# Kernel tuning notes

Hardware: AMD Instinct MI355X
Metric: run time of the kernel (lower is better)

The kernel has to match this reference:

```python
import jax, jax.numpy as jnp
import numpy as np

N, E, F, DH, R = 50000, 800000, 128, 128, 6  # nodes, edges, in-feat, hidden, relations (heads=1)
EPS = 1e-5
NEG_SLOPE = 0.01


def setup_inputs() -> dict:
    key = jax.random.key(0)
    ks = jax.random.split(key, 20)
    sF = 1.0 / np.sqrt(F)
    sD = 1.0 / np.sqrt(DH)
    return {
        "x": jax.random.normal(ks[0], (N, F), dtype=jnp.float32),
        "edge_index": jax.random.randint(ks[1], (2, E), 0, N, dtype=jnp.int64),
        "edge_type": jax.random.randint(ks[2], (E,), 0, R, dtype=jnp.int64),
        # RGCNConv params
        "rgcn_w": jax.random.normal(ks[3], (R, F, DH), dtype=jnp.float32) * sF,
        "rgcn_root": jax.random.normal(ks[4], (F, DH), dtype=jnp.float32) * sF,
        "rgcn_bias": jnp.zeros((DH,), dtype=jnp.float32),
        # TransformerConv params (heads=1, concat=True)
        "wq": jax.random.normal(ks[5], (DH, DH), dtype=jnp.float32) * sD,
        "bq": jnp.zeros((DH,), dtype=jnp.float32),
        "wk": jax.random.normal(ks[6], (DH, DH), dtype=jnp.float32) * sD,
        "bk": jnp.zeros((DH,), dtype=jnp.float32),
        "wv": jax.random.normal(ks[7], (DH, DH), dtype=jnp.float32) * sD,
        "bv": jnp.zeros((DH,), dtype=jnp.float32),
        "wskip": jax.random.normal(ks[8], (DH, DH), dtype=jnp.float32) * sD,
        "bskip": jnp.zeros((DH,), dtype=jnp.float32),
        # BatchNorm1d params (training-mode batch stats)
        "bn_gamma": jnp.ones((DH,), dtype=jnp.float32),
        "bn_beta": jnp.zeros((DH,), dtype=jnp.float32),
    }


def _rgcn(x, src, dst, edge_type, w, root, bias):
    # PyG RGCNConv: per-relation mean aggregation of x_j @ W_r over incoming edges, + root + bias
    out = x @ root + bias  # [N, DH]
    for r in range(R):
        m = (edge_type == r)
        xw = x @ w[r]  # [N, DH]
        msg = jnp.where(m[:, None], xw[src], 0.0)  # [E, DH]
        s = jax.ops.segment_sum(msg, dst, num_segments=N)
        cnt = jax.ops.segment_sum(m.astype(x.dtype), dst, num_segments=N)
        out = out + s / jnp.maximum(cnt, 1.0)[:, None]
    return out


def _transformer_conv(x, src, dst, wq, bq, wk, bk, wv, bv, wskip, bskip):
    # PyG TransformerConv, heads=1: edge-softmax attention over incoming edges + skip projection
    q = x @ wq + bq  # [N, DH]
    k = x @ wk + bk
    v = x @ wv + bv
    score = jnp.sum(q[dst] * k[src], axis=-1) / jnp.sqrt(jnp.asarray(DH, x.dtype))  # [E]
    smax = jax.ops.segment_max(score, dst, num_segments=N)  # -inf for empty segments (unused)
    a = jnp.exp(score - smax[dst])
    denom = jax.ops.segment_sum(a, dst, num_segments=N)
    alpha = a / denom[dst]  # every edge's dst has >=1 edge, denom > 0
    agg = jax.ops.segment_sum(alpha[:, None] * v[src], dst, num_segments=N)  # [N, DH]
    return agg + (x @ wskip + bskip)


def reference(x, edge_index, edge_type, rgcn_w, rgcn_root, rgcn_bias,
              wq, bq, wk, bk, wv, bv, wskip, bskip, bn_gamma, bn_beta):
    src, dst = edge_index[0], edge_index[1]
    h = _rgcn(x, src, dst, edge_type, rgcn_w, rgcn_root, rgcn_bias)
    h = _transformer_conv(h, src, dst, wq, bq, wk, bk, wv, bv, wskip, bskip)
    # BatchNorm1d (training: batch statistics, biased variance)
    mu = jnp.mean(h, axis=0)
    var = jnp.mean(jnp.square(h - mu), axis=0)
    h = bn_gamma * (h - mu) * jax.lax.rsqrt(var + EPS) + bn_beta
    return jnp.where(h > 0, h, NEG_SLOPE * h)
```

## Files before the change

kernel.cpp:

```cpp
#include <hip/hip_runtime.h>
#include <hip/hip_bf16.h>
#include <math.h>

#define FDIM 128
#define NREL 6

typedef _Float16 half8 __attribute__((ext_vector_type(8)));
typedef _Float16 h16x2 __attribute__((ext_vector_type(2)));
typedef float f32x4 __attribute__((ext_vector_type(4)));

#if __has_builtin(__builtin_amdgcn_fdot2)
#define FDOT2(A, B, C) __builtin_amdgcn_fdot2((A), (B), (C), false)
#else
#define FDOT2(A, B, C) ((float)(A)[0] * (float)(B)[0] + ((float)(A)[1] * (float)(B)[1] + (C)))
#endif

static __device__ __forceinline__ unsigned short f2h(float f) {
  union { _Float16 h; unsigned short u; } p; p.h = (_Float16)f; return p.u;
}

__global__ void cvt_x_kernel(const float* __restrict__ x, unsigned short* __restrict__ xh,
                             int n4) {
  int i = blockIdx.x * 256 + threadIdx.x;
  if (i < n4) {
    float4 v = ((const float4*)x)[i];
    union { _Float16 h[4]; uint2 u; } p;
    p.h[0] = (_Float16)v.x; p.h[1] = (_Float16)v.y;
    p.h[2] = (_Float16)v.z; p.h[3] = (_Float16)v.w;
    ((uint2*)xh)[i] = p.u;
  }
}

__global__ void cvt_wr_kernel(const float* __restrict__ root, const float* __restrict__ w,
                              unsigned short* __restrict__ bt) {
  int i = blockIdx.x * 256 + threadIdx.x;
  if (i < 896 * 128) {
    int n = i / 896, kk = i - n * 896;
    float v = (kk < 128) ? root[kk * 128 + n] : w[(long long)(kk - 128) * 128 + n];
    bt[i] = f2h(v);
  }
}

struct WPtrs { const float* W[4]; };
__global__ void cvt_wq_kernel(WPtrs wp, unsigned short* __restrict__ bt) {
  int i = blockIdx.x * 256 + threadIdx.x;
  if (i < 4 * 128 * 128) {
    int z = i >> 14;
    int r = i & 16383;
    int n = r >> 7, kk = r & 127;
    bt[i] = f2h(wp.W[z][kk * 128 + n]);
  }
}

struct GArgs {
  const unsigned short* Ax;
  const unsigned short* Aagg;
  const unsigned short* Bt;
  const float* bias[4];
  unsigned short* qh; unsigned short* kh; unsigned short* vh; float* sk;
  unsigned short* h;
  int M, K;
};

template <int MODE>
__launch_bounds__(256)
__global__ void gemm_mfma(GArgs g) {
  __shared__ unsigned short Ah[64 * 64];
  __shared__ unsigned short Bh[128 * 64];
  const int tid = threadIdx.x;
  const int lane = tid & 63;
  const int wid = tid >> 6;
  const int wm = wid >> 1, wn = wid & 1;
  const int lr = lane & 15, lk = lane >> 4;
  const int m0 = blockIdx.x * 64;
  const int z = (MODE == 1) ? blockIdx.z : 0;
  const unsigned short* Bt = g.Bt + (long long)z * 128 * g.K;
  const int K = g.K;
  const int M = g.M;

  f32x4 acc[2][4];
#pragma unroll
  for (int a = 0; a < 2; ++a)
#pragma unroll
    for (int b = 0; b < 4; ++b) { acc[a][b][0] = 0.f; acc[a][b][1] = 0.f; acc[a][b][2] = 0.f; acc[a][b][3] = 0.f; }

  for (int k0 = 0; k0 < K; k0 += 64) {
    __syncthreads();
#pragma unroll
    for (int p = 0; p < 2; ++p) {
      int idx = tid + 256 * p;
      int r = idx >> 3, c = idx & 7;
      int row = m0 + r; if (row > M - 1) row = M - 1;
      const unsigned short* srcp;
      if (MODE == 0)
        srcp = (k0 < 128) ? (g.Ax + (long long)row * 128 + k0 + c * 8)
                          : (g.Aagg + (long long)row * 768 + (k0 - 128) + c * 8);
      else
        srcp = g.Ax + (long long)row * 128 + k0 + c * 8;
      uint4 u = *(const uint4*)srcp;
      ((uint4*)Ah)[r * 8 + (c ^ (r & 7))] = u;
    }
#pragma unroll
    for (int p = 0; p < 4; ++p) {
      int idx = tid + 256 * p;
      int rn = idx >> 3, c = idx & 7;
      uint4 u = *(const uint4*)(Bt + (long long)rn * K + k0 + c * 8);
      ((uint4*)Bh)[rn * 8 + (c ^ (rn & 7))] = u;
    }
    __syncthreads();
#pragma unroll
    for (int ks = 0; ks < 2; ++ks) {
      half8 a[2], b[4];
#pragma unroll
      for (int fm = 0; fm < 2; ++fm) {
        int row = wm * 32 + fm * 16 + lr;
        a[fm] = *(const half8*)&((uint4*)Ah)[row * 8 + ((ks * 4 + lk) ^ (row & 7))];
      }
#pragma unroll
      for (int fn = 0; fn < 4; ++fn) {
        int col = wn * 64 + fn * 16 + lr;
        b[fn] = *(const half8*)&((uint4*)Bh)[col * 8 + ((ks * 4 + lk) ^ (col & 7))];
      }
#pragma unroll
      for (int fm = 0; fm < 2; ++fm)
#pragma unroll
        for (int fn = 0; fn < 4; ++fn)
          acc[fm][fn] = __builtin_amdgcn_mfma_f32_16x16x32_f16(a[fm], b[fn], acc[fm][fn], 0, 0, 0);
    }
  }

  const float CF = 0.08838834764831845f * 1.4426950408889634f;
  const float* bias = (MODE == 0) ? g.bias[0] : g.bias[z];
#pragma unroll
  for (int fm = 0; fm < 2; ++fm) {
#pragma unroll
    for (int fn = 0; fn < 4; ++fn) {
      int col = wn * 64 + fn * 16 + lr;
      float bv = bias[col];
#pragma unroll
      for (int j = 0; j < 4; ++j) {
        int row = m0 + wm * 32 + fm * 16 + lk * 4 + j;
        if (row < M) {
          float vv = acc[fm][fn][j] + bv;
          long long off = (long long)row * 128 + col;
          if (MODE == 0) {
            g.h[off] = f2h(vv);
          } else {
            if (z == 0) g.qh[off] = f2h(vv * CF);
            else if (z == 1) g.kh[off] = f2h(vv);
            else if (z == 2) g.vh[off] = f2h(vv);
            else g.sk[off] = vv;
          }
        }
      }
    }
  }
}

__global__ void hist_kernel(const int* __restrict__ dst, const int* __restrict__ etype,
                            int* __restrict__ cnt, int E) {
  int e = blockIdx.x * blockDim.x + threadIdx.x;
  if (e < E) atomicAdd(&cnt[dst[e] * NREL + etype[e]], 1);
}

__launch_bounds__(1024)
__global__ void scan1(const int* __restrict__ deg, int* __restrict__ incl,
                      int* __restrict__ part, int n) {
  __shared__ int sh[1024];
  int tid = threadIdx.x;
  int i = blockIdx.x * 1024 + tid;
  sh[tid] = (i < n) ? deg[i] : 0;
  __syncthreads();
  for (int o = 1; o < 1024; o <<= 1) {
    int t = (tid >= o) ? sh[tid - o] : 0;
    __syncthreads();
    sh[tid] += t;
    __syncthreads();
  }
  if (i < n) incl[i] = sh[tid];
  if (tid == 1023) part[blockIdx.x] = sh[1023];
}

__global__ void scan2(int* part, int nb) {
  int lane = threadIdx.x;
  int run = 0;
  for (int b0 = 0; b0 < nb; b0 += 64) {
    int i = b0 + lane;
    int orig = (i < nb) ? part[i] : 0;
    int v = orig;
#pragma unroll
    for (int o = 1; o < 64; o <<= 1) {
      int t = __shfl_up(v, o);
      if (lane >= o) v += t;
    }
    if (i < nb) part[i] = run + v - orig;
    run += __shfl(v, 63);
  }
}

__global__ void scan3(const int* __restrict__ incl, const int* __restrict__ part,
                      int* __restrict__ offs, int n) {
  int i = blockIdx.x * blockDim.x + threadIdx.x;
  if (i < n) {
    offs[i + 1] = incl[i] + part[i >> 10];
    if (i == 0) offs[0] = 0;
  }
}

__global__ void scatter_kernel(const int* __restrict__ src, const int* __restrict__ dst,
                               const int* __restrict__ etype, const int* __restrict__ offs6,
                               int* __restrict__ cur, int* __restrict__ csrc, int E) {
  int e = blockIdx.x * blockDim.x + threadIdx.x;
  if (e < E) {
    int key = dst[e] * NREL + etype[e];
    int p = offs6[key] + atomicAdd(&cur[key], 1);
    csrc[p] = src[e] << 8;
  }
}

__launch_bounds__(256)
__global__ void rgcn_agg(const unsigned short* __restrict__ xh, const int* __restrict__ offs6,
                         const int* __restrict__ csrc,
                         unsigned short* __restrict__ aggh, int N) {
  int node = blockIdx.x * 4 + (threadIdx.x >> 6);
  if (node >= N) return;
  int lane = threadIdx.x & 63;
  const char* xc = (const char*)xh;
  const int* bp = offs6 + node * NREL;
  const int b0 = bp[0];
  int bn0 = bp[1], bn1 = bp[2], bn2 = bp[3], bn3 = bp[4], bn4 = bp[5], bn5 = bp[6];
  const int b6 = bn5;
  unsigned* ap = (unsigned*)(aggh + (long long)node * (NREL * FDIM)) + lane;

  float tx = 0.f, ty = 0.f;
  float px = 0.f, py = 0.f;
  int bprev = b0, snaps = 0;

#define FLUSH(EPOS)                                                          \
  while (snaps < NREL && bn0 == (EPOS)) {                                    \
    int cnt_ = (EPOS) - bprev;                                               \
    float inv_ = cnt_ ? 1.f / (float)cnt_ : 0.f;                             \
    union { _Float16 h[2]; unsigned u; } pk_;                                \
    pk_.h[0] = (_Float16)((tx - px) * inv_);                                 \
    pk_.h[1] = (_Float16)((ty - py) * inv_);                                 \
    *ap = pk_.u; ap += 64;                                                   \
    px = tx; py = ty; bprev = (EPOS); ++snaps;                               \
    bn0 = bn1; bn1 = bn2; bn2 = bn3; bn3 = bn4; bn4 = bn5;                   \
  }

#define EAT(XU)                                                              \
  {                                                                          \
    union { unsigned u; _Float16 h[2]; } c_; c_.u = (XU);                    \
    tx += (float)c_.h[0]; ty += (float)c_.h[1];                              \
  }

  FLUSH(b0)
  int e = b0;
  for (; e + 16 <= b6; e += 16) {
    unsigned xv[16];
#pragma unroll
    for (int t = 0; t < 16; ++t)
      xv[t] = ((const unsigned*)(xc + csrc[e + t]))[lane];
    EAT(xv[0])  FLUSH(e + 1)   EAT(xv[1])  FLUSH(e + 2)
    EAT(xv[2])  FLUSH(e + 3)   EAT(xv[3])  FLUSH(e + 4)
    EAT(xv[4])  FLUSH(e + 5)   EAT(xv[5])  FLUSH(e + 6)
    EAT(xv[6])  FLUSH(e + 7)   EAT(xv[7])  FLUSH(e + 8)
    EAT(xv[8])  FLUSH(e + 9)   EAT(xv[9])  FLUSH(e + 10)
    EAT(xv[10]) FLUSH(e + 11)  EAT(xv[11]) FLUSH(e + 12)
    EAT(xv[12]) FLUSH(e + 13)  EAT(xv[13]) FLUSH(e + 14)
    EAT(xv[14]) FLUSH(e + 15)  EAT(xv[15]) FLUSH(e + 16)
  }
  for (; e + 4 <= b6; e += 4) {
    unsigned y0 = ((const unsigned*)(xc + csrc[e + 0]))[lane];
    unsigned y1 = ((const unsigned*)(xc + csrc[e + 1]))[lane];
    unsigned y2 = ((const unsigned*)(xc + csrc[e + 2]))[lane];
    unsigned y3 = ((const unsigned*)(xc + csrc[e + 3]))[lane];
    EAT(y0) FLUSH(e + 1) EAT(y1) FLUSH(e + 2)
    EAT(y2) FLUSH(e + 3) EAT(y3) FLUSH(e + 4)
  }
  for (; e < b6; ++e) {
    unsigned xv = ((const unsigned*)(xc + csrc[e]))[lane];
    EAT(xv) FLUSH(e + 1)
  }
#undef EAT
#undef FLUSH
}

__launch_bounds__(256)
__global__ void attn_kernel(const unsigned short* __restrict__ qh,
                            const unsigned short* __restrict__ kh,
                            const unsigned short* __restrict__ vh,
                            const int* __restrict__ offs6, const int* __restrict__ csrc,
                            float* __restrict__ out,
                            float* __restrict__ gsumB, float* __restrict__ gsqB, int N) {
  __shared__ float bsum[4][FDIM];
  __shared__ float bsq[4][FDIM];
  int wv = threadIdx.x >> 6;
  int node = blockIdx.x * 4 + wv;
  int lane = threadIdx.x & 63;
  bool active = (node < N);
  int start = 0, end = 0;
  if (active) { start = offs6[node * NREL]; end = offs6[node * NREL + NREL]; }
  int deg = end - start;

  const int g16 = lane >> 4;
  const int f = lane & 15;
  const char* kc = (const char*)kh;
  const char* vc = (const char*)vh;

  union U4 { uint4 u; h16x2 h[4]; };
  U4 qf;
  if (active) qf.u = *(const uint4*)(qh + (long long)node * FDIM + f * 8);

  float m = -INFINITY, den = 0.f, acc0 = 0.f, acc1 = 0.f;

#define LOADQ(E0, S0, S1, S2, S3, KU, V0, V1, V2, V3)                        \
  {                                                                          \
    S0 = csrc[(E0) + (g16 ^ 0)];                                             \
    S1 = csrc[(E0) + (g16 ^ 1)];                                             \
    S2 = csrc[(E0) + (g16 ^ 2)];                                             \
    S3 = csrc[(E0) + (g16 ^ 3)];                                             \
    KU = *(const uint4*)(kc + S0 + f * 16);                                  \
    V0 = ((const unsigned*)(vc + S0))[lane];                                 \
    V1 = ((const unsigned*)(vc + S1))[lane];                                 \
    V2 = ((const unsigned*)(vc + S2))[lane];                                 \
    V3 = ((const unsigned*)(vc + S3))[lane];                                 \
  }

#define PROCESS(KU, V0, V1, V2, V3, MASKED, M0, M1, M2, M3)                  \
  {                                                                          \
    U4 kf; kf.u = KU;                                                        \
    float pd = FDOT2(qf.h[0], kf.h[0], 0.f);                                 \
    pd = FDOT2(qf.h[1], kf.h[1], pd);                                        \
    pd = FDOT2(qf.h[2], kf.h[2], pd);                                        \
    pd = FDOT2(qf.h[3], kf.h[3], pd);                                        \
    pd += __shfl_xor(pd, 1);  pd += __shfl_xor(pd, 2);                       \
    pd += __shfl_xor(pd, 4);  pd += __shfl_xor(pd, 8);                       \
    float sc0 = pd;                                                          \
    float sc1 = __shfl_xor(pd, 16);                                          \
    float sc2 = __shfl_xor(pd, 32);                                          \
    float sc3 = __shfl_xor(pd, 48);                                          \
    if (MASKED) {                                                            \
      if (!(M0)) sc0 = -INFINITY;                                            \
      if (!(M1)) sc1 = -INFINITY;                                            \
      if (!(M2)) sc2 = -INFINITY;                                            \
      if (!(M3)) sc3 = -INFINITY;                                            \
    }                                                                        \
    float mx = fmaxf(fmaxf(sc0, sc1), fmaxf(sc2, sc3));                      \
    float mn = fmaxf(m, mx);                                                 \
    float scl = exp2f(m - mn);                                               \
    float a0 = exp2f(sc0 - mn), a1 = exp2f(sc1 - mn);                        \
    float a2 = exp2f(sc2 - mn), a3 = exp2f(sc3 - mn);                        \
    den = den * scl + ((a0 + a1) + (a2 + a3));                               \
    union { unsigned u; _Float16 h[2]; } w0, w1, w2, w3;                     \
    w0.u = V0; w1.u = V1; w2.u = V2; w3.u = V3;                              \
    acc0 = acc0 * scl + a0 * (float)w0.h[0] + a1 * (float)w1.h[0]            \
                      + a2 * (float)w2.h[0] + a3 * (float)w3.h[0];           \
    acc1 = acc1 * scl + a0 * (float)w0.h[1] + a1 * (float)w1.h[1]            \
                      + a2 * (float)w2.h[1] + a3 * (float)w3.h[1];           \
    m = mn;                                                                  \
  }

  if (deg > 0) {
    int nfull4 = deg & ~3;
    int e = start;
    if (nfull4 > 0) {
      int sA0, sA1, sA2, sA3; uint4 kA; unsigned vA0, vA1, vA2, vA3;
      LOADQ(e, sA0, sA1, sA2, sA3, kA, vA0, vA1, vA2, vA3)
      for (; e < start + nfull4; e += 4) {
        int sB0, sB1, sB2, sB3; uint4 kB; unsigned vB0, vB1, vB2, vB3;
        bool more = (e + 4 < start + nfull4);
        if (more) LOADQ(e + 4, sB0, sB1, sB2, sB3, kB, vB0, vB1, vB2, vB3)
        PROCESS(kA, vA0, vA1, vA2, vA3, false, 1, 1, 1, 1)
        if (more) { kA = kB; vA0 = vB0; vA1 = vB1; vA2 = vB2; vA3 = vB3; }
      }
    }
    int rem = deg & 3;
    if (rem) {
      int e0 = start + nfull4;
      int j0 = g16 ^ 0, j1 = g16 ^ 1, j2 = g16 ^ 2, j3 = g16 ^ 3;
      int sT0 = csrc[e0 + (j0 < rem ? j0 : 0)];
      int sT1 = csrc[e0 + (j1 < rem ? j1 : 0)];
      int sT2 = csrc[e0 + (j2 < rem ? j2 : 0)];
      int sT3 = csrc[e0 + (j3 < rem ? j3 : 0)];
      uint4 kT = *(const uint4*)(kc + sT0 + f * 16);
      unsigned vT0 = ((const unsigned*)(vc + sT0))[lane];
      unsigned vT1 = ((const unsigned*)(vc + sT1))[lane];
      unsigned vT2 = ((const unsigned*)(vc + sT2))[lane];
      unsigned vT3 = ((const unsigned*)(vc + sT3))[lane];
      PROCESS(kT, vT0, vT1, vT2, vT3, true, j0 < rem, j1 < rem, j2 < rem, j3 < rem)
    }
  }
#undef LOADQ
#undef PROCESS

  float2 o = make_float2(0.f, 0.f);
  if (active) {
    float2* op = (float2*)(out + (long long)node * FDIM);
    o = op[lane];
    if (deg > 0) {
      float inv = 1.f / den;
      o.x += acc0 * inv;
      o.y += acc1 * inv;
      op[lane] = o;
    }
  }

  ((float2*)bsum[wv])[lane] = make_float2(o.x, o.y);
  ((float2*)bsq[wv])[lane]  = make_float2(o.x * o.x, o.y * o.y);
  __syncthreads();
  if (threadIdx.x < FDIM) {
    int d = threadIdx.x;
    float s  = bsum[0][d] + bsum[1][d] + bsum[2][d] + bsum[3][d];
    float q2 = bsq[0][d]  + bsq[1][d]  + bsq[2][d]  + bsq[3][d];
    int bucket = blockIdx.x & 31;
    atomicAdd(&gsumB[bucket * FDIM + d], s);
    atomicAdd(&gsqB[bucket * FDIM + d], q2);
  }
}

__global__ void bn_final(const float* __restrict__ gsumB, const float* __restrict__ gsqB,
                         const float* __restrict__ gamma, const float* __restrict__ beta,
                         float* __restrict__ ss, int N) {
  int d = threadIdx.x;
  if (d < FDIM) {
    float s = 0.f, q = 0.f;
    for (int b = 0; b < 32; ++b) { s += gsumB[b * FDIM + d]; q += gsqB[b * FDIM + d]; }
    float mean = s / (float)N;
    float var = q / (float)N - mean * mean;
    var = fmaxf(var, 0.f);
    float sc = gamma[d] * rsqrtf(var + 1e-5f);
    ss[d] = sc;
    ss[FDIM + d] = beta[d] - mean * sc;
  }
}

__global__ void bn_apply(float* __restrict__ x, const float* __restrict__ ss, long long total4) {
  long long i = (long long)blockIdx.x * blockDim.x + threadIdx.x;
  if (i < total4) {
    int d0 = (int)((i * 4) & (FDIM - 1));
    float4 vv = ((const float4*)x)[i];
    float y0 = ss[d0 + 0] * vv.x + ss[FDIM + d0 + 0];
    float y1 = ss[d0 + 1] * vv.y + ss[FDIM + d0 + 1];
    float y2 = ss[d0 + 2] * vv.z + ss[FDIM + d0 + 2];
    float y3 = ss[d0 + 3] * vv.w + ss[FDIM + d0 + 3];
    vv.x = (y0 > 0.f) ? y0 : 0.01f * y0;
    vv.y = (y1 > 0.f) ? y1 : 0.01f * y1;
    vv.z = (y2 > 0.f) ? y2 : 0.01f * y2;
    vv.w = (y3 > 0.f) ? y3 : 0.01f * y3;
    ((float4*)x)[i] = vv;
  }
}

extern "C" void kernel_launch(void* const* d_in, const int* in_sizes, int n_in,
                              void* d_out, int out_size, void* d_ws, size_t ws_size,
                              hipStream_t stream) {
  const float* x         = (const float*)d_in[0];
  const int*   ei        = (const int*)d_in[1];
  const int*   etype     = (const int*)d_in[2];
  const float* rgcn_w    = (const float*)d_in[3];
  const float* rgcn_root = (const float*)d_in[4];
  const float* rgcn_bias = (const float*)d_in[5];
  const float* wq = (const float*)d_in[6];  const float* bq = (const float*)d_in[7];
  const float* wk = (const float*)d_in[8];  const float* bk = (const float*)d_in[9];
  const float* wv = (const float*)d_in[10]; const float* bv = (const float*)d_in[11];
  const float* wsk = (const float*)d_in[12]; const float* bsk = (const float*)d_in[13];
  const float* gamma = (const float*)d_in[14]; const float* beta = (const float*)d_in[15];

  const int N = in_sizes[0] / FDIM;
  const int E = in_sizes[1] / 2;
  const int* src = ei;
  const int* dst = ei + E;
  const int NK = N * NREL;

  char* base = (char*)d_ws;
  size_t off = 0;
  auto alloc = [&](size_t bytes) -> char* {
    char* p = base + off;
    off += (bytes + 255) & ~(size_t)255;
    return p;
  };
  unsigned short* aggh = (unsigned short*)alloc((size_t)N * (NREL * FDIM) * 2);
  unsigned short* qbuf = aggh;
  unsigned short* kbuf = aggh + (size_t)N * FDIM;
  unsigned short* vbuf = aggh + 2 * (size_t)N * FDIM;
  unsigned short* xh   = (unsigned short*)alloc((size_t)N * FDIM * 2);
  unsigned short* hh   = (unsigned short*)alloc((size_t)N * FDIM * 2);
  unsigned short* btR  = (unsigned short*)alloc((size_t)896 * 128 * 2);
  unsigned short* btQ  = (unsigned short*)alloc((size_t)4 * 128 * 128 * 2);
  int* cnt6 = (int*)alloc((size_t)2 * NK * 4);
  int* cur  = cnt6 + NK;
  int* offs6 = (int*)alloc((size_t)(NK + 1) * 4);
  int* incl = (int*)alloc((size_t)NK * 4);
  int* part = (int*)alloc((size_t)512 * 4);
  int* csrc = (int*)alloc((size_t)E * 4);
  float* gsumB = (float*)alloc((size_t)32 * FDIM * 4);
  float* gsqB  = (float*)alloc((size_t)32 * FDIM * 4);
  float* ss    = (float*)alloc((size_t)2 * FDIM * 4);

  float* out = (float*)d_out;

  hipMemsetAsync(cnt6, 0, (size_t)2 * NK * sizeof(int), stream);
  hipMemsetAsync(gsumB, 0, (size_t)64 * FDIM * sizeof(float), stream);

  int n4 = N * FDIM / 4;
  cvt_x_kernel<<<(n4 + 255) / 256, 256, 0, stream>>>(x, xh, n4);
  cvt_wr_kernel<<<(896 * 128 + 255) / 256, 256, 0, stream>>>(rgcn_root, rgcn_w, btR);
  WPtrs wp; wp.W[0] = wq; wp.W[1] = wk; wp.W[2] = wv; wp.W[3] = wsk;
  cvt_wq_kernel<<<(4 * 128 * 128 + 255) / 256, 256, 0, stream>>>(wp, btQ);

  hist_kernel<<<(E + 255) / 256, 256, 0, stream>>>(dst, etype, cnt6, E);
  int nb = (NK + 1023) / 1024;
  scan1<<<nb, 1024, 0, stream>>>(cnt6, incl, part, NK);
  scan2<<<1, 64, 0, stream>>>(part, nb);
  scan3<<<(NK + 255) / 256, 256, 0, stream>>>(incl, part, offs6, NK);
  scatter_kernel<<<(E + 255) / 256, 256, 0, stream>>>(src, dst, etype, offs6, cur, csrc, E);

  const int nodeBlocks = (N + 3) / 4;
  const int gemmBlocks = (N + 63) / 64;

  rgcn_agg<<<nodeBlocks, 256, 0, stream>>>(xh, offs6, csrc, aggh, N);

  GArgs g0 = {};
  g0.Ax = xh; g0.Aagg = aggh; g0.Bt = btR;
  g0.bias[0] = rgcn_bias;
  g0.h = hh; g0.M = N; g0.K = 896;
  gemm_mfma<0><<<dim3(gemmBlocks, 1, 1), 256, 0, stream>>>(g0);

  GArgs g1 = {};
  g1.Ax = hh; g1.Bt = btQ;
  g1.bias[0] = bq; g1.bias[1] = bk; g1.bias[2] = bv; g1.bias[3] = bsk;
  g1.qh = qbuf; g1.kh = kbuf; g1.vh = vbuf; g1.sk = out;
  g1.M = N; g1.K = 128;
  gemm_mfma<1><<<dim3(gemmBlocks, 1, 4), 256, 0, stream>>>(g1);

  attn_kernel<<<nodeBlocks, 256, 0, stream>>>(qbuf, kbuf, vbuf, offs6, csrc, out,
                                              gsumB, gsqB, N);

  bn_final<<<1, 128, 0, stream>>>(gsumB, gsqB, gamma, beta, ss, N);
  long long total4 = (long long)N * FDIM / 4;
  bn_apply<<<(int)((total4 + 255) / 256), 256, 0, stream>>>(out, ss, total4);
}
```

Baseline: 305.2 us.

## Interleave K and V rows, merge weight conversions, use fp16 attention accumulation

K and V projections are written into one interleaved buffer with 512-byte rows, so each gathered source node's key and value sit in the same memory region. The three conversion kernels are merged into one launch. The CSR source list now stores raw indices, and each consumer shifts them to its own row stride. The attention value accumulator switches from two fp32 scalars to a packed fp16 pair, which cuts ALU work at the cost of accuracy and a possible overflow risk in the running sum.

```diff
diff --git a/kernel.cpp b/kernel.cpp
--- a/kernel.cpp
+++ b/kernel.cpp
@@ -19,36 +19,34 @@
   union { _Float16 h; unsigned short u; } p; p.h = (_Float16)f; return p.u;
 }
 
-__global__ void cvt_x_kernel(const float* __restrict__ x, unsigned short* __restrict__ xh,
-                             int n4) {
+struct WPtrs { const float* W[4]; };
+
+__global__ void cvt_all_kernel(const float* __restrict__ x, unsigned short* __restrict__ xh,
+                               const float* __restrict__ root, const float* __restrict__ w,
+                               unsigned short* __restrict__ btR,
+                               WPtrs wp, unsigned short* __restrict__ btQ, int n4x) {
   int i = blockIdx.x * 256 + threadIdx.x;
-  if (i < n4) {
+  if (i < n4x) {
     float4 v = ((const float4*)x)[i];
     union { _Float16 h[4]; uint2 u; } p;
     p.h[0] = (_Float16)v.x; p.h[1] = (_Float16)v.y;
     p.h[2] = (_Float16)v.z; p.h[3] = (_Float16)v.w;
     ((uint2*)xh)[i] = p.u;
-  }
-}
-
-__global__ void cvt_wr_kernel(const float* __restrict__ root, const float* __restrict__ w,
-                              unsigned short* __restrict__ bt) {
-  int i = blockIdx.x * 256 + threadIdx.x;
-  if (i < 896 * 128) {
-    int n = i / 896, kk = i - n * 896;
+    return;
+  }
+  int j = i - n4x;
+  if (j < 896 * 128) {
+    int n = j / 896, kk = j - n * 896;
     float v = (kk < 128) ? root[kk * 128 + n] : w[(long long)(kk - 128) * 128 + n];
-    bt[i] = f2h(v);
-  }
-}
-
-struct WPtrs { const float* W[4]; };
-__global__ void cvt_wq_kernel(WPtrs wp, unsigned short* __restrict__ bt) {
-  int i = blockIdx.x * 256 + threadIdx.x;
-  if (i < 4 * 128 * 128) {
-    int z = i >> 14;
-    int r = i & 16383;
+    btR[j] = f2h(v);
+    return;
+  }
+  int q = j - 896 * 128;
+  if (q < 4 * 128 * 128) {
+    int z = q >> 14;
+    int r = q & 16383;
     int n = r >> 7, kk = r & 127;
-    bt[i] = f2h(wp.W[z][kk * 128 + n]);
+    btQ[q] = f2h(wp.W[z][kk * 128 + n]);
   }
 }
 
@@ -57,7 +55,7 @@
   const unsigned short* Aagg;
   const unsigned short* Bt;
   const float* bias[4];
-  unsigned short* qh; unsigned short* kh; unsigned short* vh; float* sk;
+  unsigned short* qh; unsigned short* kv; float* sk;
   unsigned short* h;
   int M, K;
 };
@@ -142,14 +140,13 @@
         int row = m0 + wm * 32 + fm * 16 + lk * 4 + j;
         if (row < M) {
           float vv = acc[fm][fn][j] + bv;
-          long long off = (long long)row * 128 + col;
           if (MODE == 0) {
-            g.h[off] = f2h(vv);
+            g.h[(long long)row * 128 + col] = f2h(vv);
           } else {
-            if (z == 0) g.qh[off] = f2h(vv * CF);
-            else if (z == 1) g.kh[off] = f2h(vv);
-            else if (z == 2) g.vh[off] = f2h(vv);
-            else g.sk[off] = vv;
+            if (z == 0) g.qh[(long long)row * 128 + col] = f2h(vv * CF);
+            else if (z == 1) g.kv[(long long)row * 256 + col] = f2h(vv);
+            else if (z == 2) g.kv[(long long)row * 256 + 128 + col] = f2h(vv);
+            else g.sk[(long long)row * 128 + col] = vv;
           }
         }
       }
@@ -214,7 +211,7 @@
   if (e < E) {
     int key = dst[e] * NREL + etype[e];
     int p = offs6[key] + atomicAdd(&cur[key], 1);
-    csrc[p] = src[e] << 8;
+    csrc[p] = src[e];
   }
 }
 
@@ -260,7 +257,7 @@
     unsigned xv[16];
 #pragma unroll
     for (int t = 0; t < 16; ++t)
-      xv[t] = ((const unsigned*)(xc + csrc[e + t]))[lane];
+      xv[t] = ((const unsigned*)(xc + ((long long)csrc[e + t] << 8)))[lane];
     EAT(xv[0])  FLUSH(e + 1)   EAT(xv[1])  FLUSH(e + 2)
     EAT(xv[2])  FLUSH(e + 3)   EAT(xv[3])  FLUSH(e + 4)
     EAT(xv[4])  FLUSH(e + 5)   EAT(xv[5])  FLUSH(e + 6)
@@ -271,15 +268,15 @@
     EAT(xv[14]) FLUSH(e + 15)  EAT(xv[15]) FLUSH(e + 16)
   }
   for (; e + 4 <= b6; e += 4) {
-    unsigned y0 = ((const unsigned*)(xc + csrc[e + 0]))[lane];
-    unsigned y1 = ((const unsigned*)(xc + csrc[e + 1]))[lane];
-    unsigned y2 = ((const unsigned*)(xc + csrc[e + 2]))[lane];
-    unsigned y3 = ((const unsigned*)(xc + csrc[e + 3]))[lane];
+    unsigned y0 = ((const unsigned*)(xc + ((long long)csrc[e + 0] << 8)))[lane];
+    unsigned y1 = ((const unsigned*)(xc + ((long long)csrc[e + 1] << 8)))[lane];
+    unsigned y2 = ((const unsigned*)(xc + ((long long)csrc[e + 2] << 8)))[lane];
+    unsigned y3 = ((const unsigned*)(xc + ((long long)csrc[e + 3] << 8)))[lane];
     EAT(y0) FLUSH(e + 1) EAT(y1) FLUSH(e + 2)
     EAT(y2) FLUSH(e + 3) EAT(y3) FLUSH(e + 4)
   }
   for (; e < b6; ++e) {
-    unsigned xv = ((const unsigned*)(xc + csrc[e]))[lane];
+    unsigned xv = ((const unsigned*)(xc + ((long long)csrc[e] << 8)))[lane];
     EAT(xv) FLUSH(e + 1)
   }
 #undef EAT
@@ -288,8 +285,7 @@
 
 __launch_bounds__(256)
 __global__ void attn_kernel(const unsigned short* __restrict__ qh,
-                            const unsigned short* __restrict__ kh,
-                            const unsigned short* __restrict__ vh,
+                            const unsigned short* __restrict__ kv,
                             const int* __restrict__ offs6, const int* __restrict__ csrc,
                             float* __restrict__ out,
                             float* __restrict__ gsumB, float* __restrict__ gsqB, int N) {
@@ -305,26 +301,26 @@
 
   const int g16 = lane >> 4;
   const int f = lane & 15;
-  const char* kc = (const char*)kh;
-  const char* vc = (const char*)vh;
+  const char* kvc = (const char*)kv;
 
   union U4 { uint4 u; h16x2 h[4]; };
   U4 qf;
   if (active) qf.u = *(const uint4*)(qh + (long long)node * FDIM + f * 8);
 
-  float m = -INFINITY, den = 0.f, acc0 = 0.f, acc1 = 0.f;
-
-#define LOADQ(E0, S0, S1, S2, S3, KU, V0, V1, V2, V3)                        \
+  float m = -INFINITY, den = 0.f;
+  h16x2 accv; accv[0] = (_Float16)0.f; accv[1] = (_Float16)0.f;
+
+#define LOADQ(E0, KU, V0, V1, V2, V3)                                        \
   {                                                                          \
-    S0 = csrc[(E0) + (g16 ^ 0)];                                             \
-    S1 = csrc[(E0) + (g16 ^ 1)];                                             \
-    S2 = csrc[(E0) + (g16 ^ 2)];                                             \
-    S3 = csrc[(E0) + (g16 ^ 3)];                                             \
-    KU = *(const uint4*)(kc + S0 + f * 16);                                  \
-    V0 = ((const unsigned*)(vc + S0))[lane];                                 \
-    V1 = ((const unsigned*)(vc + S1))[lane];                                 \
-    V2 = ((const unsigned*)(vc + S2))[lane];                                 \
-    V3 = ((const unsigned*)(vc + S3))[lane];                                 \
+    long long S0 = (long long)csrc[(E0) + (g16 ^ 0)] << 9;                   \
+    long long S1 = (long long)csrc[(E0) + (g16 ^ 1)] << 9;                   \
+    long long S2 = (long long)csrc[(E0) + (g16 ^ 2)] << 9;                   \
+    long long S3 = (long long)csrc[(E0) + (g16 ^ 3)] << 9;                   \
+    KU = *(const uint4*)(kvc + S0 + f * 16);                                 \
+    V0 = *(const unsigned*)(kvc + S0 + 256 + lane * 4);                      \
+    V1 = *(const unsigned*)(kvc + S1 + 256 + lane * 4);                      \
+    V2 = *(const unsigned*)(kvc + S2 + 256 + lane * 4);                      \
+    V3 = *(const unsigned*)(kvc + S3 + 256 + lane * 4);                      \
   }
 
 #define PROCESS(KU, V0, V1, V2, V3, MASKED, M0, M1, M2, M3)                  \
@@ -352,12 +348,14 @@
     float a0 = exp2f(sc0 - mn), a1 = exp2f(sc1 - mn);                        \
     float a2 = exp2f(sc2 - mn), a3 = exp2f(sc3 - mn);                        \
     den = den * scl + ((a0 + a1) + (a2 + a3));                               \
-    union { unsigned u; _Float16 h[2]; } w0, w1, w2, w3;                     \
+    union { unsigned u; h16x2 h; } w0, w1, w2, w3;                           \
     w0.u = V0; w1.u = V1; w2.u = V2; w3.u = V3;                              \
-    acc0 = acc0 * scl + a0 * (float)w0.h[0] + a1 * (float)w1.h[0]            \
-                      + a2 * (float)w2.h[0] + a3 * (float)w3.h[0];           \
-    acc1 = acc1 * scl + a0 * (float)w0.h[1] + a1 * (float)w1.h[1]            \
-                      + a2 * (float)w2.h[1] + a3 * (float)w3.h[1];           \
+    h16x2 sclh; sclh[0] = (_Float16)scl; sclh[1] = sclh[0];                  \
+    h16x2 ah; accv = accv * sclh;                                            \
+    ah[0] = (_Float16)a0; ah[1] = ah[0]; accv += ah * w0.h;                  \
+    ah[0] = (_Float16)a1; ah[1] = ah[0]; accv += ah * w1.h;                  \
+    ah[0] = (_Float16)a2; ah[1] = ah[0]; accv += ah * w2.h;                  \
+    ah[0] = (_Float16)a3; ah[1] = ah[0]; accv += ah * w3.h;                  \
     m = mn;                                                                  \
   }
 
@@ -365,12 +363,12 @@
     int nfull4 = deg & ~3;
     int e = start;
     if (nfull4 > 0) {
-      int sA0, sA1, sA2, sA3; uint4 kA; unsigned vA0, vA1, vA2, vA3;
-      LOADQ(e, sA0, sA1, sA2, sA3, kA, vA0, vA1, vA2, vA3)
+      uint4 kA; unsigned vA0, vA1, vA2, vA3;
+      LOADQ(e, kA, vA0, vA1, vA2, vA3)
       for (; e < start + nfull4; e += 4) {
-        int sB0, sB1, sB2, sB3; uint4 kB; unsigned vB0, vB1, vB2, vB3;
+        uint4 kB; unsigned vB0, vB1, vB2, vB3;
         bool more = (e + 4 < start + nfull4);
-        if (more) LOADQ(e + 4, sB0, sB1, sB2, sB3, kB, vB0, vB1, vB2, vB3)
+        if (more) LOADQ(e + 4, kB, vB0, vB1, vB2, vB3)
         PROCESS(kA, vA0, vA1, vA2, vA3, false, 1, 1, 1, 1)
         if (more) { kA = kB; vA0 = vB0; vA1 = vB1; vA2 = vB2; vA3 = vB3; }
       }
@@ -379,15 +377,15 @@
     if (rem) {
       int e0 = start + nfull4;
       int j0 = g16 ^ 0, j1 = g16 ^ 1, j2 = g16 ^ 2, j3 = g16 ^ 3;
-      int sT0 = csrc[e0 + (j0 < rem ? j0 : 0)];
-      int sT1 = csrc[e0 + (j1 < rem ? j1 : 0)];
-      int sT2 = csrc[e0 + (j2 < rem ? j2 : 0)];
-      int sT3 = csrc[e0 + (j3 < rem ? j3 : 0)];
-      uint4 kT = *(const uint4*)(kc + sT0 + f * 16);
-      unsigned vT0 = ((const unsigned*)(vc + sT0))[lane];
-      unsigned vT1 = ((const unsigned*)(vc + sT1))[lane];
-      unsigned vT2 = ((const unsigned*)(vc + sT2))[lane];
-      unsigned vT3 = ((const unsigned*)(vc + sT3))[lane];
+      long long sT0 = (long long)csrc[e0 + (j0 < rem ? j0 : 0)] << 9;
+      long long sT1 = (long long)csrc[e0 + (j1 < rem ? j1 : 0)] << 9;
+      long long sT2 = (long long)csrc[e0 + (j2 < rem ? j2 : 0)] << 9;
+      long long sT3 = (long long)csrc[e0 + (j3 < rem ? j3 : 0)] << 9;
+      uint4 kT = *(const uint4*)(kvc + sT0 + f * 16);
+      unsigned vT0 = *(const unsigned*)(kvc + sT0 + 256 + lane * 4);
+      unsigned vT1 = *(const unsigned*)(kvc + sT1 + 256 + lane * 4);
+      unsigned vT2 = *(const unsigned*)(kvc + sT2 + 256 + lane * 4);
+      unsigned vT3 = *(const unsigned*)(kvc + sT3 + 256 + lane * 4);
       PROCESS(kT, vT0, vT1, vT2, vT3, true, j0 < rem, j1 < rem, j2 < rem, j3 < rem)
     }
   }
@@ -400,8 +398,8 @@
     o = op[lane];
     if (deg > 0) {
       float inv = 1.f / den;
-      o.x += acc0 * inv;
-      o.y += acc1 * inv;
+      o.x += (float)accv[0] * inv;
+      o.y += (float)accv[1] * inv;
       op[lane] = o;
     }
   }
@@ -481,9 +479,8 @@
     return p;
   };
   unsigned short* aggh = (unsigned short*)alloc((size_t)N * (NREL * FDIM) * 2);
-  unsigned short* qbuf = aggh;
-  unsigned short* kbuf = aggh + (size_t)N * FDIM;
-  unsigned short* vbuf = aggh + 2 * (size_t)N * FDIM;
+  unsigned short* qbuf  = aggh;
+  unsigned short* kvbuf = aggh + (size_t)N * FDIM;
   unsigned short* xh   = (unsigned short*)alloc((size_t)N * FDIM * 2);
   unsigned short* hh   = (unsigned short*)alloc((size_t)N * FDIM * 2);
   unsigned short* btR  = (unsigned short*)alloc((size_t)896 * 128 * 2);
@@ -503,11 +500,11 @@
   hipMemsetAsync(cnt6, 0, (size_t)2 * NK * sizeof(int), stream);
   hipMemsetAsync(gsumB, 0, (size_t)64 * FDIM * sizeof(float), stream);
 
-  int n4 = N * FDIM / 4;
-  cvt_x_kernel<<<(n4 + 255) / 256, 256, 0, stream>>>(x, xh, n4);
-  cvt_wr_kernel<<<(896 * 128 + 255) / 256, 256, 0, stream>>>(rgcn_root, rgcn_w, btR);
+  int n4x = N * FDIM / 4;
   WPtrs wp; wp.W[0] = wq; wp.W[1] = wk; wp.W[2] = wv; wp.W[3] = wsk;
-  cvt_wq_kernel<<<(4 * 128 * 128 + 255) / 256, 256, 0, stream>>>(wp, btQ);
+  int cvtTotal = n4x + 896 * 128 + 4 * 128 * 128;
+  cvt_all_kernel<<<(cvtTotal + 255) / 256, 256, 0, stream>>>(
+      x, xh, rgcn_root, rgcn_w, btR, wp, btQ, n4x);
 
   hist_kernel<<<(E + 255) / 256, 256, 0, stream>>>(dst, etype, cnt6, E);
   int nb = (NK + 1023) / 1024;
@@ -530,11 +527,11 @@
   GArgs g1 = {};
   g1.Ax = hh; g1.Bt = btQ;
   g1.bias[0] = bq; g1.bias[1] = bk; g1.bias[2] = bv; g1.bias[3] = bsk;
-  g1.qh = qbuf; g1.kh = kbuf; g1.vh = vbuf; g1.sk = out;
+  g1.qh = qbuf; g1.kv = kvbuf; g1.sk = out;
   g1.M = N; g1.K = 128;
   gemm_mfma<1><<<dim3(gemmBlocks, 1, 4), 256, 0, stream>>>(g1);
 
-  attn_kernel<<<nodeBlocks, 256, 0, stream>>>(qbuf, kbuf, vbuf, offs6, csrc, out,
+  attn_kernel<<<nodeBlocks, 256, 0, stream>>>(qbuf, kvbuf, offs6, csrc, out,
                                               gsumB, gsqB, N);
 
   bn_final<<<1, 128, 0, stream>>>(gsumB, gsqB, gamma, beta, ss, N);
```

New measurement: 301.1 us, median of 2. About the same (-1.4%).
